# Kernel tuning notes

Measured on AMD Instinct MI355X. Metric: run time of the kernel, lower is better.

## Reference

```python
import jax, jax.numpy as jnp
import numpy as np

# ---- config (CSA layer, layer_idx=0 of pattern 'CSA,HCA') ----
B, T, C = 2, 2048, 2048
NH, NKV = 16, 8
HD = C // NH            # 128 head dim
ROPE_DIM = HD // 2      # partial RoPE dims (rope_head_dim=0 default)
RATIO = 4               # csa_compress_ratio
G = T // RATIO          # compressed groups (T divisible by ratio -> no pad)
IDX_NH = NH
IDX_HD = max(8, C // NH // 2)  # 64
TOPK = 64               # index_topk
Q_RANK = C // 2         # _default_rank
O_RPG = C // 2          # o_proj rank_per_group, o_groups=1


def rms_norm(x, eps=1e-6):
    return x * jax.lax.rsqrt(jnp.mean(jnp.square(x), axis=-1, keepdims=True) + eps)


def _rope(x, cos, sin):
    d = x.shape[-1] // 2
    x1, x2 = x[..., :d], x[..., d:]
    return jnp.concatenate([x1 * cos + x2 * sin, -x1 * sin + x2 * cos], axis=-1)


def partial_rope(x, cos, sin):
    # rotate only the last ROPE_DIM dims; cos/sin: [..., ROPE_DIM//2]
    xn, xr = x[..., :-ROPE_DIM], x[..., -ROPE_DIM:]
    return jnp.concatenate([xn, _rope(xr, cos, sin)], axis=-1)


def setup_inputs() -> dict:
    key = jax.random.key(0)
    ks = jax.random.split(key, 16)
    s = 0.02
    x = jax.random.normal(ks[0], (B, T, C), jnp.float32)
    pos = jnp.arange(T, dtype=jnp.float32)
    inv = 10000.0 ** (-jnp.arange(0, HD // 2, dtype=jnp.float32) / (HD // 2))
    ang = pos[:, None] * inv[None, :]  # [T, HD//2]
    p = lambda i, shp: jax.random.normal(ks[i], shp, jnp.float32) * s
    return dict(
        x=x, cos=jnp.cos(ang), sin=jnp.sin(ang),
        q_a_w=p(1, (C, Q_RANK)), q_b_w=p(2, (Q_RANK, NH * HD)),
        ck_w=p(3, (C, NKV * HD)), cv_w=p(4, (C, NKV * HD)), cg_w=p(5, (C, NKV * HD)),
        c_ape=p(6, (RATIO, NKV, HD)),
        iq_w=p(7, (C, IDX_NH * IDX_HD)), ik_w=p(8, (C, IDX_NH * IDX_HD)),
        ig_w=p(9, (C, IDX_NH * IDX_HD)), i_ape=p(10, (RATIO, IDX_NH, IDX_HD)),
        sink=jnp.zeros((NH,), jnp.float32),
        o_wa=p(11, (1, O_RPG, C)), o_pb=p(12, (O_RPG, C)),
    )


def reference(x, cos, sin, q_a_w, q_b_w, ck_w, cv_w, cg_w, c_ape,
              iq_w, ik_w, ig_w, i_ape, sink, o_wa, o_pb):
    NEG = jnp.finfo(jnp.float32).min
    half = ROPE_DIM // 2
    # --- low-rank queries + partial RoPE ---
    q = (x @ q_a_w @ q_b_w).reshape(B, T, NH, HD)
    q = partial_rope(q, cos[None, :, None, :half], sin[None, :, None, :half])
    # --- GatedCompressor: learned gated pooling over blocks of RATIO ---
    k = (x @ ck_w).reshape(B, G, RATIO, NKV, HD)
    v = (x @ cv_w).reshape(B, G, RATIO, NKV, HD)
    g = (x @ cg_w).reshape(B, G, RATIO, NKV, HD) + c_ape[None, None]
    w = jax.nn.softmax(g, axis=2)
    ck = (k * w).sum(2)  # [B,G,NKV,HD]
    cv = (v * w).sum(2)
    group_ends = jnp.arange(RATIO - 1, T, RATIO)  # [G]
    ckr = partial_rope(ck, cos[group_ends][None, :, None, :half],
                       sin[group_ends][None, :, None, :half])
    # --- LightningIndexer: compressed indexer keys + per-token top-k groups ---
    ik = (x @ ik_w).reshape(B, G, RATIO, IDX_NH, IDX_HD)
    ig = (x @ ig_w).reshape(B, G, RATIO, IDX_NH, IDX_HD) + i_ape[None, None]
    iw = jax.nn.softmax(ig, axis=2)
    ikeys = rms_norm((ik * iw).sum(2))  # [B,G,IH,IHD]
    iq = rms_norm((x @ iq_w).reshape(B, T, IDX_NH, IDX_HD))
    iscore = jnp.einsum('bthd,bghd->bhtg', iq, ikeys) * IDX_HD ** -0.5
    iscore = iscore.mean(axis=1)  # [B,T,G]
    causal = group_ends[None, None, :] <= jnp.arange(T)[None, :, None]
    iscore = jnp.where(causal, iscore, NEG)
    sel = jax.lax.top_k(iscore, TOPK)[1]  # [B,T,K]
    bidx = jnp.arange(B)[:, None, None]
    tidx = jnp.arange(T)[None, :, None]
    mask = jnp.zeros((B, T, G), bool).at[bidx, tidx, sel].set(True) & causal
    # --- compressed sparse attention with sink, GQA expand ---
    rep = NH // NKV
    kk = jnp.repeat(ckr, rep, axis=2)  # [B,G,NH,HD]
    vv = jnp.repeat(cv, rep, axis=2)
    scores = jnp.einsum('bthd,bghd->bhtg', q, kk) * HD ** -0.5
    scores = jnp.where(mask[:, None], scores, NEG)
    sinkb = jnp.broadcast_to(sink.reshape(1, NH, 1, 1), (B, NH, T, 1))
    probs = jax.nn.softmax(jnp.concatenate([scores, sinkb], axis=-1), axis=-1)[..., :-1]
    out = jnp.einsum('bhtg,bghd->bthd', probs, vv).reshape(B, T, C)
    # --- GroupedOutputProjection (o_groups=1) ---
    h = jnp.einsum('btgd,grd->btgr', out.reshape(B, T, 1, C), o_wa).reshape(B, T, -1)
    return rms_norm(h) @ o_pb
```

## Files before the change

### kernel.cpp

```cpp
#include <hip/hip_runtime.h>
#include <hip/hip_bf16.h>
#include <math.h>

constexpr int Bn  = 2;
constexpr int Tn  = 2048;
constexpr int NHn = 16;
constexpr int NKVn= 8;
constexpr int Gn  = 512;
constexpr int TKn = 64;

typedef __attribute__((ext_vector_type(8))) __bf16 bf16x8;
typedef __attribute__((ext_vector_type(4))) __bf16 bf16x4;
typedef __attribute__((ext_vector_type(2))) __bf16 bf16x2;
typedef __attribute__((ext_vector_type(4))) float f32x4;

__device__ __forceinline__ void gload_lds16(const void* g, void* l) {
  __builtin_amdgcn_global_load_lds(
      (const __attribute__((address_space(1))) unsigned int*)g,
      (__attribute__((address_space(3))) unsigned int*)l, 16, 0, 0);
}

__global__ __launch_bounds__(512) void gemm_kvqa_8ph(
    const __bf16* __restrict__ A, const __bf16* __restrict__ Bt,
    float* __restrict__ Cf, __bf16* __restrict__ Cq)
{
  constexpr int K = 2048;
  constexpr int NT = K / 64;
  __shared__ __bf16 lds[2][2][2][256][32];
  const int tid = threadIdx.x;
  const int wid = tid >> 6, lane = tid & 63;
  const int wm = wid >> 2, wn = wid & 3;
  const int row0 = blockIdx.y * 256, col0 = blockIdx.x * 256;

  f32x4 acc[8][4];
  const f32x4 zero = {0.f, 0.f, 0.f, 0.f};
  #pragma unroll
  for (int i = 0; i < 8; ++i)
    #pragma unroll
    for (int j = 0; j < 4; ++j) acc[i][j] = zero;

  auto stage1 = [&](int kt, int op, int ph, int buf) {
    long k0 = (long)kt * 64 + ph * 32;
    const __bf16* src = op ? Bt : A;
    const int base0 = op ? col0 : row0;
    #pragma unroll
    for (int l = 0; l < 2; ++l) {
      int u = l * 512 + tid;
      int r = u >> 2, c4 = u & 3;
      long csrc = (long)((c4 ^ ((r >> 1) & 3)) * 8);
      gload_lds16(src + (long)(base0 + r) * K + k0 + csrc, &lds[buf][op][ph][r][c4 * 8]);
    }
  };

  stage1(0, 0, 0, 0);
  stage1(0, 1, 0, 0);
  stage1(0, 0, 1, 0);
  stage1(0, 1, 1, 0);
  asm volatile("s_waitcnt vmcnt(4)" ::: "memory");
  asm volatile("s_barrier" ::: "memory");

  for (int kt = 0; kt < NT; ++kt) {
    const int buf = kt & 1;
    const bool pre = (kt + 1 < NT);
    bf16x8 afA[4], afB[4], bf[4];

    #pragma unroll
    for (int i = 0; i < 4; ++i) {
      int r = wm * 128 + i * 16 + (lane & 15);
      int c4 = (lane >> 4) ^ ((r >> 1) & 3);
      afA[i] = *(const bf16x8*)&lds[buf][0][0][r][c4 * 8];
    }
    #pragma unroll
    for (int i = 0; i < 4; ++i) {
      int r = wn * 64 + i * 16 + (lane & 15);
      int c4 = (lane >> 4) ^ ((r >> 1) & 3);
      bf[i] = *(const bf16x8*)&lds[buf][1][0][r][c4 * 8];
    }
    if (pre) stage1(kt + 1, 0, 0, buf ^ 1);
    asm volatile("s_barrier" ::: "memory");
    asm volatile("s_waitcnt lgkmcnt(0)" ::: "memory");
    __builtin_amdgcn_sched_barrier(0);
    __builtin_amdgcn_s_setprio(1);
    #pragma unroll
    for (int i = 0; i < 4; ++i)
      #pragma unroll
      for (int j = 0; j < 4; ++j)
        acc[i][j] = __builtin_amdgcn_mfma_f32_16x16x32_bf16(afA[i], bf[j], acc[i][j], 0, 0, 0);
    __builtin_amdgcn_s_setprio(0);
    asm volatile("s_barrier" ::: "memory");

    #pragma unroll
    for (int i = 0; i < 4; ++i) {
      int r = wm * 128 + (i + 4) * 16 + (lane & 15);
      int c4 = (lane >> 4) ^ ((r >> 1) & 3);
      afB[i] = *(const bf16x8*)&lds[buf][0][0][r][c4 * 8];
    }
    if (pre) {
      stage1(kt + 1, 1, 0, buf ^ 1);
      asm volatile("s_waitcnt vmcnt(4)" ::: "memory");
    } else {
      asm volatile("s_waitcnt vmcnt(0)" ::: "memory");
    }
    asm volatile("s_barrier" ::: "memory");
    asm volatile("s_waitcnt lgkmcnt(0)" ::: "memory");
    __builtin_amdgcn_sched_barrier(0);
    __builtin_amdgcn_s_setprio(1);
    #pragma unroll
    for (int i = 0; i < 4; ++i)
      #pragma unroll
      for (int j = 0; j < 4; ++j)
        acc[i + 4][j] = __builtin_amdgcn_mfma_f32_16x16x32_bf16(afB[i], bf[j], acc[i + 4][j], 0, 0, 0);
    __builtin_amdgcn_s_setprio(0);
    asm volatile("s_barrier" ::: "memory");

    #pragma unroll
    for (int i = 0; i < 4; ++i) {
      int r = wm * 128 + i * 16 + (lane & 15);
      int c4 = (lane >> 4) ^ ((r >> 1) & 3);
      afA[i] = *(const bf16x8*)&lds[buf][0][1][r][c4 * 8];
    }
    #pragma unroll
    for (int i = 0; i < 4; ++i) {
      int r = wn * 64 + i * 16 + (lane & 15);
      int c4 = (lane >> 4) ^ ((r >> 1) & 3);
      bf[i] = *(const bf16x8*)&lds[buf][1][1][r][c4 * 8];
    }
    if (pre) stage1(kt + 1, 0, 1, buf ^ 1);
    asm volatile("s_barrier" ::: "memory");
    asm volatile("s_waitcnt lgkmcnt(0)" ::: "memory");
    __builtin_amdgcn_sched_barrier(0);
    __builtin_amdgcn_s_setprio(1);
    #pragma unroll
    for (int i = 0; i < 4; ++i)
      #pragma unroll
      for (int j = 0; j < 4; ++j)
        acc[i][j] = __builtin_amdgcn_mfma_f32_16x16x32_bf16(afA[i], bf[j], acc[i][j], 0, 0, 0);
    __builtin_amdgcn_s_setprio(0);
    asm volatile("s_barrier" ::: "memory");

    #pragma unroll
    for (int i = 0; i < 4; ++i) {
      int r = wm * 128 + (i + 4) * 16 + (lane & 15);
      int c4 = (lane >> 4) ^ ((r >> 1) & 3);
      afB[i] = *(const bf16x8*)&lds[buf][0][1][r][c4 * 8];
    }
    if (pre) {
      stage1(kt + 1, 1, 1, buf ^ 1);
      asm volatile("s_waitcnt vmcnt(4)" ::: "memory");
    }
    asm volatile("s_barrier" ::: "memory");
    asm volatile("s_waitcnt lgkmcnt(0)" ::: "memory");
    __builtin_amdgcn_sched_barrier(0);
    __builtin_amdgcn_s_setprio(1);
    #pragma unroll
    for (int i = 0; i < 4; ++i)
      #pragma unroll
      for (int j = 0; j < 4; ++j)
        acc[i + 4][j] = __builtin_amdgcn_mfma_f32_16x16x32_bf16(afB[i], bf[j], acc[i + 4][j], 0, 0, 0);
    __builtin_amdgcn_s_setprio(0);
    asm volatile("s_barrier" ::: "memory");
  }

  const int crow = (lane >> 4) * 4, ccol = lane & 15;
  const bool isQ = (col0 >= 3072);
  #pragma unroll
  for (int mf = 0; mf < 8; ++mf)
    #pragma unroll
    for (int nf = 0; nf < 4; ++nf)
      #pragma unroll
      for (int j = 0; j < 4; ++j) {
        long r = row0 + wm * 128 + mf * 16 + crow + j;
        long c = col0 + wn * 64 + nf * 16 + ccol;
        float v = acc[mf][nf][j];
        if (isQ) Cq[r * 1024 + (c - 3072)] = (__bf16)v;
        else     Cf[r * 3072 + c] = v;
      }
}

__global__ __launch_bounds__(512) void gemm_split_8ph(
    const __bf16* __restrict__ Ah, const __bf16* __restrict__ Al,
    const __bf16* __restrict__ Bh, const __bf16* __restrict__ Bl,
    float* __restrict__ C, int M, int N, int K, float alpha)
{
  const int NT = K >> 5;
  constexpr int LA_H = 0;
  constexpr int LA_L = 8192;
  constexpr int LB_H = 16384;
  constexpr int LBUF = 28672;
  __shared__ __bf16 sm[2 * LBUF];
  const int tid = threadIdx.x;
  const int wid = tid >> 6, lane = tid & 63;
  const int wm = wid >> 2, wn = wid & 3;
  const int row0 = blockIdx.y * 256, col0 = blockIdx.x * 192;

  f32x4 acc[8][3];
  const f32x4 zero = {0.f, 0.f, 0.f, 0.f};
  #pragma unroll
  for (int i = 0; i < 8; ++i)
    #pragma unroll
    for (int j = 0; j < 3; ++j) acc[i][j] = zero;

  auto stageA = [&](int kt, int buf, int which) {
    long k0 = (long)kt * 32;
    const __bf16* src = which ? Al : Ah;
    __bf16* dst = &sm[buf * LBUF + (which ? LA_L : LA_H)];
    #pragma unroll
    for (int l = 0; l < 2; ++l) {
      int u = l * 512 + tid;
      int r = u >> 2, c4 = u & 3;
      long csrc = (long)((c4 ^ ((r >> 1) & 3)) * 8);
      gload_lds16(src + (long)(row0 + r) * K + k0 + csrc, dst + u * 8);
    }
  };
  auto stageB = [&](int kt, int buf) {
    long k0 = (long)kt * 32;
    __bf16* dst = &sm[buf * LBUF + LB_H];
    #pragma unroll
    for (int l = 0; l < 3; ++l) {
      int u = l * 512 + tid;
      int v = (u < 768) ? u : u - 768;
      const __bf16* src = (u < 768) ? Bh : Bl;
      int r = v >> 2, c4 = v & 3;
      long csrc = (long)((c4 ^ ((r >> 1) & 3)) * 8);
      gload_lds16(src + (long)(col0 + r) * K + k0 + csrc, dst + u * 8);
    }
  };

  stageB(0, 0);
  stageA(0, 0, 0);
  stageA(0, 0, 1);
  asm volatile("s_waitcnt vmcnt(2)" ::: "memory");
  asm volatile("s_barrier" ::: "memory");

  for (int kt = 0; kt < NT; ++kt) {
    const int buf = kt & 1;
    const bool pre = (kt + 1 < NT);
    bf16x8 a_h[4], a_l[4], b_h[3], b_l[3];

    #pragma unroll
    for (int i = 0; i < 4; ++i) {
      int r = wm * 128 + i * 16 + (lane & 15);
      int c4 = (lane >> 4) ^ ((r >> 1) & 3);
      a_h[i] = *(const bf16x8*)&sm[buf * LBUF + LA_H + r * 32 + c4 * 8];
    }
    #pragma unroll
    for (int j = 0; j < 3; ++j) {
      int r = wn * 48 + j * 16 + (lane & 15);
      int c4 = (lane >> 4) ^ ((r >> 1) & 3);
      b_h[j] = *(const bf16x8*)&sm[buf * LBUF + LB_H + r * 32 + c4 * 8];
    }
    if (pre) {
      stageB(kt + 1, buf ^ 1);
      asm volatile("s_waitcnt vmcnt(3)" ::: "memory");
    } else {
      asm volatile("s_waitcnt vmcnt(0)" ::: "memory");
    }
    asm volatile("s_barrier" ::: "memory");
    asm volatile("s_waitcnt lgkmcnt(0)" ::: "memory");
    __builtin_amdgcn_sched_barrier(0);
    __builtin_amdgcn_s_setprio(1);
    #pragma unroll
    for (int i = 0; i < 4; ++i)
      #pragma unroll
      for (int j = 0; j < 3; ++j)
        acc[i][j] = __builtin_amdgcn_mfma_f32_16x16x32_bf16(a_h[i], b_h[j], acc[i][j], 0, 0, 0);
    __builtin_amdgcn_s_setprio(0);
    asm volatile("s_barrier" ::: "memory");

    #pragma unroll
    for (int i = 0; i < 4; ++i) {
      int r = wm * 128 + i * 16 + (lane & 15);
      int c4 = (lane >> 4) ^ ((r >> 1) & 3);
      a_l[i] = *(const bf16x8*)&sm[buf * LBUF + LA_L + r * 32 + c4 * 8];
    }
    #pragma unroll
    for (int j = 0; j < 3; ++j) {
      int r = wn * 48 + j * 16 + (lane & 15);
      int c4 = (lane >> 4) ^ ((r >> 1) & 3);
      b_l[j] = *(const bf16x8*)&sm[buf * LBUF + LB_H + 6144 + r * 32 + c4 * 8];
    }
    if (pre) stageA(kt + 1, buf ^ 1, 0);
    asm volatile("s_barrier" ::: "memory");
    asm volatile("s_waitcnt lgkmcnt(0)" ::: "memory");
    __builtin_amdgcn_sched_barrier(0);
    __builtin_amdgcn_s_setprio(1);
    #pragma unroll
    for (int i = 0; i < 4; ++i)
      #pragma unroll
      for (int j = 0; j < 3; ++j) {
        acc[i][j] = __builtin_amdgcn_mfma_f32_16x16x32_bf16(a_h[i], b_l[j], acc[i][j], 0, 0, 0);
        acc[i][j] = __builtin_amdgcn_mfma_f32_16x16x32_bf16(a_l[i], b_h[j], acc[i][j], 0, 0, 0);
      }
    __builtin_amdgcn_s_setprio(0);
    asm volatile("s_barrier" ::: "memory");

    #pragma unroll
    for (int i = 0; i < 4; ++i) {
      int r = wm * 128 + (i + 4) * 16 + (lane & 15);
      int c4 = (lane >> 4) ^ ((r >> 1) & 3);
      a_h[i] = *(const bf16x8*)&sm[buf * LBUF + LA_H + r * 32 + c4 * 8];
    }
    if (pre) stageA(kt + 1, buf ^ 1, 1);
    asm volatile("s_barrier" ::: "memory");
    asm volatile("s_waitcnt lgkmcnt(0)" ::: "memory");
    __builtin_amdgcn_sched_barrier(0);
    __builtin_amdgcn_s_setprio(1);
    #pragma unroll
    for (int i = 0; i < 4; ++i)
      #pragma unroll
      for (int j = 0; j < 3; ++j)
        acc[i + 4][j] = __builtin_amdgcn_mfma_f32_16x16x32_bf16(a_h[i], b_h[j], acc[i + 4][j], 0, 0, 0);
    __builtin_amdgcn_s_setprio(0);
    asm volatile("s_barrier" ::: "memory");

    #pragma unroll
    for (int i = 0; i < 4; ++i) {
      int r = wm * 128 + (i + 4) * 16 + (lane & 15);
      int c4 = (lane >> 4) ^ ((r >> 1) & 3);
      a_l[i] = *(const bf16x8*)&sm[buf * LBUF + LA_L + r * 32 + c4 * 8];
    }
    if (pre)
      asm volatile("s_waitcnt vmcnt(2)" ::: "memory");
    asm volatile("s_barrier" ::: "memory");
    asm volatile("s_waitcnt lgkmcnt(0)" ::: "memory");
    __builtin_amdgcn_sched_barrier(0);
    __builtin_amdgcn_s_setprio(1);
    #pragma unroll
    for (int i = 0; i < 4; ++i)
      #pragma unroll
      for (int j = 0; j < 3; ++j) {
        acc[i + 4][j] = __builtin_amdgcn_mfma_f32_16x16x32_bf16(a_h[i], b_l[j], acc[i + 4][j], 0, 0, 0);
        acc[i + 4][j] = __builtin_amdgcn_mfma_f32_16x16x32_bf16(a_l[i], b_h[j], acc[i + 4][j], 0, 0, 0);
      }
    __builtin_amdgcn_s_setprio(0);
    asm volatile("s_barrier" ::: "memory");
  }

  const int crow = (lane >> 4) * 4, ccol = lane & 15;
  #pragma unroll
  for (int mf = 0; mf < 8; ++mf)
    #pragma unroll
    for (int nf = 0; nf < 3; ++nf)
      #pragma unroll
      for (int j = 0; j < 4; ++j) {
        long r = row0 + wm * 128 + mf * 16 + crow + j;
        long c = col0 + wn * 48 + nf * 16 + ccol;
        C[r * N + c] = acc[mf][nf][j] * alpha;
      }
}

template<int EPI>
__global__ __launch_bounds__(256) void gemm_pipe(
    const __bf16* __restrict__ A, const __bf16* __restrict__ Bt,
    void* __restrict__ Cp, int N, int K,
    const float* __restrict__ cosb, const float* __restrict__ sinb,
    const float* __restrict__ rs)
{
  const int NT = K >> 6;
  __shared__ __bf16 lds[2][2][2][128][32];
  const int tid = threadIdx.x;
  const int wid = tid >> 6, lane = tid & 63;
  const int wm = wid >> 1, wn = wid & 1;
  const int row0 = blockIdx.y * 128, col0 = blockIdx.x * 128;

  f32x4 acc[4][4];
  const f32x4 zero = {0.f, 0.f, 0.f, 0.f};
  #pragma unroll
  for (int i = 0; i < 4; ++i)
    #pragma unroll
    for (int j = 0; j < 4; ++j) acc[i][j] = zero;

  auto stage = [&](int kt, int p, int buf) {
    long k0 = (long)kt * 64 + p * 32;
    #pragma unroll
    for (int l = 0; l < 2; ++l) {
      int u = l * 256 + tid;
      int r = u >> 2, c4 = u & 3;
      long csrc = (long)((c4 ^ ((r >> 1) & 3)) * 8);
      gload_lds16(A  + (long)(row0 + r) * K + k0 + csrc, &lds[buf][0][p][r][c4 * 8]);
      gload_lds16(Bt + (long)(col0 + r) * K + k0 + csrc, &lds[buf][1][p][r][c4 * 8]);
    }
  };

  stage(0, 0, 0);
  stage(0, 1, 0);

  for (int kt = 0; kt < NT; ++kt) {
    const int buf = kt & 1;
    #pragma unroll
    for (int ph = 0; ph < 2; ++ph) {
      if (kt + 1 < NT) {
        stage(kt + 1, ph, buf ^ 1);
        asm volatile("s_waitcnt vmcnt(8)" ::: "memory");
      } else {
        if (ph == 0) asm volatile("s_waitcnt vmcnt(4)" ::: "memory");
        else         asm volatile("s_waitcnt vmcnt(0)" ::: "memory");
      }
      asm volatile("s_barrier" ::: "memory");
      bf16x8 af[4], bfr[4];
      #pragma unroll
      for (int mf = 0; mf < 4; ++mf) {
        int r = wm * 64 + mf * 16 + (lane & 15);
        int c4 = (lane >> 4) ^ ((r >> 1) & 3);
        af[mf] = *(const bf16x8*)&lds[buf][0][ph][r][c4 * 8];
      }
      #pragma unroll
      for (int nf = 0; nf < 4; ++nf) {
        int r = wn * 64 + nf * 16 + (lane & 15);
        int c4 = (lane >> 4) ^ ((r >> 1) & 3);
        bfr[nf] = *(const bf16x8*)&lds[buf][1][ph][r][c4 * 8];
      }
      __builtin_amdgcn_s_setprio(1);
      #pragma unroll
      for (int mf = 0; mf < 4; ++mf)
        #pragma unroll
        for (int nf = 0; nf < 4; ++nf)
          acc[mf][nf] = __builtin_amdgcn_mfma_f32_16x16x32_bf16(af[mf], bfr[nf], acc[mf][nf], 0, 0, 0);
      __builtin_amdgcn_s_setprio(0);
      asm volatile("s_barrier" ::: "memory");
    }
  }

  const int crow = (lane >> 4) * 4, ccol = lane & 15;
  if constexpr (EPI == 1) {
    __bf16* C = (__bf16*)Cp;
    if (wn == 1) {
      #pragma unroll
      for (int mf = 0; mf < 4; ++mf)
        #pragma unroll
        for (int j = 0; j < 4; ++j) {
          long r = row0 + wm * 64 + mf * 16 + crow + j;
          int t = (int)(r & 2047);
          #pragma unroll
          for (int nfp = 0; nfp < 2; ++nfp) {
            int jj = nfp * 16 + ccol;
            float c = cosb[t * 64 + jj], s = sinb[t * 64 + jj];
            float x1 = acc[mf][nfp][j];
            float x2 = acc[mf][nfp + 2][j];
            C[r * N + col0 + 64 + jj] = (__bf16)(x1 * c + x2 * s);
            C[r * N + col0 + 96 + jj] = (__bf16)(-x1 * s + x2 * c);
          }
        }
    } else {
      #pragma unroll
      for (int mf = 0; mf < 4; ++mf)
        #pragma unroll
        for (int nf = 0; nf < 4; ++nf)
          #pragma unroll
          for (int j = 0; j < 4; ++j) {
            long r = row0 + wm * 64 + mf * 16 + crow + j;
            long c = col0 + nf * 16 + ccol;
            C[r * N + c] = (__bf16)acc[mf][nf][j];
          }
    }
  } else {
    #pragma unroll
    for (int mf = 0; mf < 4; ++mf)
      #pragma unroll
      for (int nf = 0; nf < 4; ++nf)
        #pragma unroll
        for (int j = 0; j < 4; ++j) {
          long r = row0 + wm * 64 + mf * 16 + crow + j;
          long c = col0 + wn * 64 + nf * 16 + ccol;
          float v = acc[mf][nf][j];
          if constexpr (EPI == 2)
            ((float*)Cp)[r * N + c] = v * rs[r];
          else
            ((__bf16*)Cp)[r * N + c] = (__bf16)v;
        }
  }
}

__global__ __launch_bounds__(256) void gemm_split(
    const __bf16* __restrict__ Ah, const __bf16* __restrict__ Al,
    const __bf16* __restrict__ Bh, const __bf16* __restrict__ Bl,
    float* __restrict__ C, int M, int N, int K, float alpha,
    long sA, long sB, long sC)
{
  const int NT = K >> 5;
  __shared__ __bf16 lds[2][4][128][32];
  const int tid = threadIdx.x;
  const int wid = tid >> 6, lane = tid & 63;
  const int wm = wid >> 1, wn = wid & 1;
  const int row0 = blockIdx.y * 128, col0 = blockIdx.x * 128;
  Ah += (long)blockIdx.z * sA;  Al += (long)blockIdx.z * sA;
  Bh += (long)blockIdx.z * sB;  Bl += (long)blockIdx.z * sB;

  f32x4 acc[4][4];
  const f32x4 zero = {0.f, 0.f, 0.f, 0.f};
  #pragma unroll
  for (int i = 0; i < 4; ++i)
    #pragma unroll
    for (int j = 0; j < 4; ++j) acc[i][j] = zero;

  auto stage = [&](int kt, int buf) {
    long k0 = (long)kt * 32;
    #pragma unroll
    for (int l = 0; l < 2; ++l) {
      int u = l * 256 + tid;
      int r = u >> 2, c4 = u & 3;
      long csrc = (long)((c4 ^ ((r >> 1) & 3)) * 8);
      long ga = (long)(row0 + r) * K + k0 + csrc;
      long gb = (long)(col0 + r) * K + k0 + csrc;
      gload_lds16(Ah + ga, &lds[buf][0][r][c4 * 8]);
      gload_lds16(Al + ga, &lds[buf][1][r][c4 * 8]);
      gload_lds16(Bh + gb, &lds[buf][2][r][c4 * 8]);
      gload_lds16(Bl + gb, &lds[buf][3][r][c4 * 8]);
    }
  };

  stage(0, 0);

  for (int kt = 0; kt < NT; ++kt) {
    const int buf = kt & 1;
    if (kt + 1 < NT) {
      stage(kt + 1, buf ^ 1);
      asm volatile("s_waitcnt vmcnt(8)" ::: "memory");
    } else {
      asm volatile("s_waitcnt vmcnt(0)" ::: "memory");
    }
    asm volatile("s_barrier" ::: "memory");
    bf16x8 ah[4], al[4], bh[4], bl[4];
    #pragma unroll
    for (int mf = 0; mf < 4; ++mf) {
      int r = wm * 64 + mf * 16 + (lane & 15);
      int c4 = (lane >> 4) ^ ((r >> 1) & 3);
      ah[mf] = *(const bf16x8*)&lds[buf][0][r][c4 * 8];
      al[mf] = *(const bf16x8*)&lds[buf][1][r][c4 * 8];
    }
    #pragma unroll
    for (int nf = 0; nf < 4; ++nf) {
      int r = wn * 64 + nf * 16 + (lane & 15);
      int c4 = (lane >> 4) ^ ((r >> 1) & 3);
      bh[nf] = *(const bf16x8*)&lds[buf][2][r][c4 * 8];
      bl[nf] = *(const bf16x8*)&lds[buf][3][r][c4 * 8];
    }
    __builtin_amdgcn_s_setprio(1);
    #pragma unroll
    for (int mf = 0; mf < 4; ++mf)
      #pragma unroll
      for (int nf = 0; nf < 4; ++nf) {
        acc[mf][nf] = __builtin_amdgcn_mfma_f32_16x16x32_bf16(ah[mf], bh[nf], acc[mf][nf], 0, 0, 0);
        acc[mf][nf] = __builtin_amdgcn_mfma_f32_16x16x32_bf16(ah[mf], bl[nf], acc[mf][nf], 0, 0, 0);
        acc[mf][nf] = __builtin_amdgcn_mfma_f32_16x16x32_bf16(al[mf], bh[nf], acc[mf][nf], 0, 0, 0);
      }
    __builtin_amdgcn_s_setprio(0);
    asm volatile("s_barrier" ::: "memory");
  }

  const int crow = (lane >> 4) * 4, ccol = lane & 15;
  #pragma unroll
  for (int mf = 0; mf < 4; ++mf)
    #pragma unroll
    for (int nf = 0; nf < 4; ++nf)
      #pragma unroll
      for (int j = 0; j < 4; ++j) {
        long r = row0 + wm * 64 + mf * 16 + crow + j;
        long c = col0 + wn * 64 + nf * 16 + ccol;
        C[(long)blockIdx.z * sC + r * N + c] = acc[mf][nf][j] * alpha;
      }
}

__global__ __launch_bounds__(256) void prep_index(
    const float* __restrict__ x,
    const float* __restrict__ s0, const float* __restrict__ s1,
    const float* __restrict__ s2,
    __bf16* __restrict__ hiB, __bf16* __restrict__ loB, long dstride,
    __bf16* __restrict__ xhi, __bf16* __restrict__ xlo)
{
  __shared__ float tile[64][65];
  int z = blockIdx.y;
  int tid = threadIdx.x;
  if (z < 3) {
    const int R = 2048, Cc = 1024;
    const float* in = (z == 0) ? s0 : (z == 1) ? s1 : s2;
    __bf16* hiT = hiB + (long)z * dstride;
    __bf16* loT = loB + (long)z * dstride;
    int f = blockIdx.x;
    int r0 = (f >> 4) * 64, c0 = (f & 15) * 64;
    #pragma unroll
    for (int j = 0; j < 16; ++j) {
      int idx = tid + j * 256;
      int r = idx >> 6, c = idx & 63;
      tile[r][c] = in[(long)(r0 + r) * Cc + c0 + c];
    }
    __syncthreads();
    #pragma unroll
    for (int j = 0; j < 16; ++j) {
      int idx = tid + j * 256;
      int c = idx >> 6, r = idx & 63;
      float v = tile[r][c];
      __bf16 h = (__bf16)v;
      hiT[(long)(c0 + c) * R + r0 + r] = h;
      loT[(long)(c0 + c) * R + r0 + r] = (__bf16)(v - (float)h);
    }
  } else {
    for (long i = ((long)blockIdx.x * 256 + tid) * 4; i < 8388608; i += 524288) {
      float4 v = *(const float4*)&x[i];
      bf16x4 h, l;
      h[0] = (__bf16)v.x; l[0] = (__bf16)(v.x - (float)h[0]);
      h[1] = (__bf16)v.y; l[1] = (__bf16)(v.y - (float)h[1]);
      h[2] = (__bf16)v.z; l[2] = (__bf16)(v.z - (float)h[2]);
      h[3] = (__bf16)v.w; l[3] = (__bf16)(v.w - (float)h[3]);
      *(bf16x4*)&xhi[i] = h;
      *(bf16x4*)&xlo[i] = l;
    }
  }
}

__global__ __launch_bounds__(256) void prep_main(
    const float* __restrict__ s0, const float* __restrict__ s1,
    const float* __restrict__ s2, const float* __restrict__ s3,
    const float* __restrict__ s4, const float* __restrict__ s5,
    const float* __restrict__ wa,
    __bf16* __restrict__ W, long W2, __bf16* __restrict__ owab)
{
  __shared__ float tile[64][65];
  int z = blockIdx.y;
  int tid = threadIdx.x;
  if (z < 6) {
    int R, Cc, r0, c0;
    const float* in;
    if (z < 4) {
      R = 2048; Cc = 1024;
      in = (z == 0) ? s0 : (z == 1) ? s1 : (z == 2) ? s2 : s3;
      r0 = (blockIdx.x >> 4) * 64; c0 = (blockIdx.x & 15) * 64;
    } else {
      R = 1024; Cc = 2048;
      in = (z == 4) ? s4 : s5;
      r0 = (blockIdx.x >> 5) * 64; c0 = (blockIdx.x & 31) * 64;
    }
    __bf16* out = W + (long)z * W2;
    #pragma unroll
    for (int j = 0; j < 16; ++j) {
      int idx = tid + j * 256;
      int r = idx >> 6, c = idx & 63;
      tile[r][c] = in[(long)(r0 + r) * Cc + c0 + c];
    }
    __syncthreads();
    #pragma unroll
    for (int j = 0; j < 16; ++j) {
      int idx = tid + j * 256;
      int c = idx >> 6, r = idx & 63;
      out[(long)(c0 + c) * R + r0 + r] = (__bf16)tile[r][c];
    }
  } else {
    for (long i = ((long)blockIdx.x * 256 + tid) * 4; i < 2097152; i += 524288) {
      float4 v = *(const float4*)&wa[i];
      bf16x4 o;
      o[0] = (__bf16)v.x; o[1] = (__bf16)v.y; o[2] = (__bf16)v.z; o[3] = (__bf16)v.w;
      *(bf16x4*)&owab[i] = o;
    }
  }
}

__global__ __launch_bounds__(256) void reduce_ckcv(
    const float* __restrict__ base, const float* __restrict__ c_ape,
    const float* __restrict__ cosb, const float* __restrict__ sinb,
    __bf16* __restrict__ ckb, __bf16* __restrict__ cvb)
{
  __shared__ float sck[256];
  const long S = 3072;
  int tid = threadIdx.x;
  int c = blockIdx.x * 256 + tid;
  int g = blockIdx.y, b = blockIdx.z;
  long row0 = (long)b * Tn + 4 * g;
  float lg[4], mx = -1e30f;
  #pragma unroll
  for (int r = 0; r < 4; ++r) {
    lg[r] = base[(row0 + r) * S + 2048 + c] + c_ape[r * 1024 + c];
    mx = fmaxf(mx, lg[r]);
  }
  float ssum = 0.f;
  #pragma unroll
  for (int r = 0; r < 4; ++r) { lg[r] = expf(lg[r] - mx); ssum += lg[r]; }
  float inv = 1.f / ssum, ak = 0.f, av = 0.f;
  #pragma unroll
  for (int r = 0; r < 4; ++r) {
    float w = lg[r] * inv;
    ak = fmaf(base[(row0 + r) * S + c],        w, ak);
    av = fmaf(base[(row0 + r) * S + 1024 + c], w, av);
  }
  long o = ((long)b * Gn + g) * 1024 + c;
  cvb[o] = (__bf16)av;
  sck[tid] = ak;
  __syncthreads();
  int d = c & 127;
  float outk = ak;
  if (d >= 64) {
    int t = 4 * g + 3;
    if (d < 96) {
      int j = d - 64;
      outk = ak * cosb[t * 64 + j] + sck[tid + 32] * sinb[t * 64 + j];
    } else {
      int j = d - 96;
      outk = -sck[tid - 32] * sinb[t * 64 + j] + ak * cosb[t * 64 + j];
    }
  }
  ckb[o] = (__bf16)outk;
}

__global__ __launch_bounds__(1024) void reduce_idx_fused(
    const float* __restrict__ base, const float* __restrict__ i_ape,
    __bf16* __restrict__ khi, __bf16* __restrict__ klo,
    __bf16* __restrict__ qhi, __bf16* __restrict__ qlo)
{
  const long S = 3072;
  int tid = threadIdx.x;
  int bid = blockIdx.x;
  if (bid < Gn * Bn) {
    int g = bid & (Gn - 1), b = bid >> 9;
    long row0 = (long)b * Tn + 4 * g;
    float lg[4], mx = -1e30f;
    #pragma unroll
    for (int r = 0; r < 4; ++r) {
      lg[r] = base[(row0 + r) * S + 1024 + tid] + i_ape[r * 1024 + tid];
      mx = fmaxf(mx, lg[r]);
    }
    float ssum = 0.f;
    #pragma unroll
    for (int r = 0; r < 4; ++r) { lg[r] = expf(lg[r] - mx); ssum += lg[r]; }
    float inv = 1.f / ssum, red = 0.f;
    #pragma unroll
    for (int r = 0; r < 4; ++r) red = fmaf(base[(row0 + r) * S + tid], lg[r] * inv, red);
    float ss = red * red;
    #pragma unroll
    for (int o = 32; o; o >>= 1) ss += __shfl_xor(ss, o);
    float v = red * rsqrtf(ss * (1.f / 64.f) + 1e-6f);
    long oi = ((long)b * Gn + g) * 1024 + tid;
    __bf16 h = (__bf16)v;
    khi[oi] = h; klo[oi] = (__bf16)(v - (float)h);
  } else {
    long row = bid - Gn * Bn;
    float v = base[row * S + 2048 + tid];
    float ss = v * v;
    #pragma unroll
    for (int o = 32; o; o >>= 1) ss += __shfl_xor(ss, o);
    float y = v * rsqrtf(ss * (1.f / 64.f) + 1e-6f);
    __bf16 h = (__bf16)y;
    qhi[row * 1024 + tid] = h;
    qlo[row * 1024 + tid] = (__bf16)(y - (float)h);
  }
}

__global__ __launch_bounds__(256) void rms_scales(
    const __bf16* __restrict__ h, float* __restrict__ rs)
{
  int wid = threadIdx.x >> 6, lane = threadIdx.x & 63;
  long row = (long)blockIdx.x * 4 + wid;
  const __bf16* hr = h + row * 1024 + lane * 16;
  bf16x8 a = *(const bf16x8*)hr;
  bf16x8 b = *(const bf16x8*)(hr + 8);
  float ss = 0.f;
  #pragma unroll
  for (int j = 0; j < 8; ++j) {
    float x = (float)a[j], y = (float)b[j];
    ss = fmaf(x, x, ss); ss = fmaf(y, y, ss);
  }
  #pragma unroll
  for (int o = 1; o < 64; o <<= 1) ss += __shfl_xor(ss, o);
  if (lane == 0) rs[row] = rsqrtf(ss * (1.f / 1024.f) + 1e-6f);
}

__global__ __launch_bounds__(256) void topk_kernel(
    const float* __restrict__ iscore, int* __restrict__ selidx, int* __restrict__ selcnt)
{
  int wave = threadIdx.x >> 6, lane = threadIdx.x & 63;
  long bt = (long)blockIdx.x * 4 + wave;
  int t = (int)(bt % Tn);
  const float* row = iscore + bt * Gn;
  int ng = (t + 1) >> 2; if (ng > Gn) ng = Gn;
  int cap = ng < TKn ? ng : TKn;
  float s[8];
  #pragma unroll
  for (int j = 0; j < 8; ++j) {
    int g = lane + 64 * j;
    s[j] = (g < ng) ? row[g] : -INFINITY;
  }
  int* outp = selidx + bt * TKn;
  for (int it = 0; it < cap; ++it) {
    float bv = -INFINITY; int bi = Gn;
    #pragma unroll
    for (int j = 0; j < 8; ++j) {
      int g = lane + 64 * j;
      if (s[j] > bv) { bv = s[j]; bi = g; }
    }
    #pragma unroll
    for (int o = 1; o < 64; o <<= 1) {
      float ov = __shfl_xor(bv, o); int oi = __shfl_xor(bi, o);
      if (ov > bv || (ov == bv && oi < bi)) { bv = ov; bi = oi; }
    }
    if (lane == 0) outp[it] = bi;
    #pragma unroll
    for (int j = 0; j < 8; ++j) if (bi == lane + 64 * j) s[j] = -INFINITY;
  }
  for (int it = cap + lane; it < TKn; it += 64) outp[it] = 0;
  if (lane == 0) selcnt[bt] = cap;
}

__global__ __launch_bounds__(256) void attn_kernel(
    const __bf16* __restrict__ q, const __bf16* __restrict__ ckb,
    const __bf16* __restrict__ cvb, const int* __restrict__ selidx,
    const int* __restrict__ selcnt, const float* __restrict__ sink,
    __bf16* __restrict__ out)
{
  __shared__ float sS[4][16][68];
  __shared__ int   sG[4][64];
  const float scale = 0.08838834764831845f;
  int wid = threadIdx.x >> 6, lane = threadIdx.x & 63;
  long bt = (long)blockIdx.x * 4 + wid;
  int b = (int)(bt >> 11);
  int cnt = selcnt[bt];
  int gid = (lane < cnt) ? selidx[bt * TKn + lane] : 0;
  sG[wid][lane] = gid;

  int grp = lane >> 3;
  int sub = lane & 7;
  int h0 = grp * 2, h1 = h0 + 1;
  int d0 = sub * 16;

  const __bf16* qrow = q + bt * 2048;
  float q0[16], q1[16];
  {
    bf16x8 a0 = *(const bf16x8*)&qrow[h0 * 128 + d0];
    bf16x8 a1 = *(const bf16x8*)&qrow[h0 * 128 + d0 + 8];
    bf16x8 c0 = *(const bf16x8*)&qrow[h1 * 128 + d0];
    bf16x8 c1 = *(const bf16x8*)&qrow[h1 * 128 + d0 + 8];
    #pragma unroll
    for (int j = 0; j < 8; ++j) {
      q0[j] = (float)a0[j]; q0[8 + j] = (float)a1[j];
      q1[j] = (float)c0[j]; q1[8 + j] = (float)c1[j];
    }
  }
  __syncthreads();

  for (int i0 = 0; i0 < 64; i0 += 8) {
    #pragma unroll
    for (int u = 0; u < 8; ++u) {
      int i = i0 + u;
      int g = sG[wid][i];
      const __bf16* kr = ckb + ((long)(b * Gn + g)) * 1024 + lane * 16;
      bf16x8 k0 = *(const bf16x8*)kr;
      bf16x8 k1 = *(const bf16x8*)(kr + 8);
      float p0 = 0.f, p1 = 0.f;
      #pragma unroll
      for (int j = 0; j < 8; ++j) {
        float kv = (float)k0[j];
        p0 = fmaf(kv, q0[j], p0); p1 = fmaf(kv, q1[j], p1);
      }
      #pragma unroll
      for (int j = 0; j < 8; ++j) {
        float kv = (float)k1[j];
        p0 = fmaf(kv, q0[8 + j], p0); p1 = fmaf(kv, q1[8 + j], p1);
      }
      p0 += __shfl_xor(p0, 1); p0 += __shfl_xor(p0, 2); p0 += __shfl_xor(p0, 4);
      p1 += __shfl_xor(p1, 1); p1 += __shfl_xor(p1, 2); p1 += __shfl_xor(p1, 4);
      if (sub == 0) { sS[wid][h0][i] = p0; sS[wid][h1][i] = p1; }
    }
  }
  __syncthreads();

  {
    int h = lane >> 2, qtr = lane & 3;
    float sv[16];
    float mx = -INFINITY;
    #pragma unroll
    for (int j = 0; j < 16; ++j) {
      int i = qtr * 16 + j;
      float s = (i < cnt) ? sS[wid][h][i] * scale : -INFINITY;
      sv[j] = s; mx = fmaxf(mx, s);
    }
    mx = fmaxf(mx, __shfl_xor(mx, 1));
    mx = fmaxf(mx, __shfl_xor(mx, 2));
    float snk = sink[h];
    mx = fmaxf(mx, snk);
    float sum = 0.f;
    #pragma unroll
    for (int j = 0; j < 16; ++j) { sv[j] = __expf(sv[j] - mx); sum += sv[j]; }
    sum += __shfl_xor(sum, 1);
    sum += __shfl_xor(sum, 2);
    sum += __expf(snk - mx);
    float inv = 1.f / sum;
    #pragma unroll
    for (int j = 0; j < 16; ++j) sS[wid][h][qtr * 16 + j] = sv[j] * inv;
  }
  __syncthreads();

  float o0[16], o1[16];
  #pragma unroll
  for (int j = 0; j < 16; ++j) { o0[j] = 0.f; o1[j] = 0.f; }
  for (int i0 = 0; i0 < 64; i0 += 8) {
    #pragma unroll
    for (int u = 0; u < 8; ++u) {
      int i = i0 + u;
      int g = sG[wid][i];
      float p0 = sS[wid][h0][i], p1 = sS[wid][h1][i];
      const __bf16* vr = cvb + ((long)(b * Gn + g)) * 1024 + lane * 16;
      bf16x8 v0 = *(const bf16x8*)vr;
      bf16x8 v1 = *(const bf16x8*)(vr + 8);
      #pragma unroll
      for (int j = 0; j < 8; ++j) {
        float vv = (float)v0[j];
        o0[j] = fmaf(p0, vv, o0[j]); o1[j] = fmaf(p1, vv, o1[j]);
      }
      #pragma unroll
      for (int j = 0; j < 8; ++j) {
        float vv = (float)v1[j];
        o0[8 + j] = fmaf(p0, vv, o0[8 + j]); o1[8 + j] = fmaf(p1, vv, o1[8 + j]);
      }
    }
  }
  __bf16* ob = out + bt * 2048;
  bf16x8 w;
  #pragma unroll
  for (int j = 0; j < 8; ++j) w[j] = (__bf16)o0[j];
  *(bf16x8*)&ob[h0 * 128 + d0] = w;
  #pragma unroll
  for (int j = 0; j < 8; ++j) w[j] = (__bf16)o0[8 + j];
  *(bf16x8*)&ob[h0 * 128 + d0 + 8] = w;
  #pragma unroll
  for (int j = 0; j < 8; ++j) w[j] = (__bf16)o1[j];
  *(bf16x8*)&ob[h1 * 128 + d0] = w;
  #pragma unroll
  for (int j = 0; j < 8; ++j) w[j] = (__bf16)o1[8 + j];
  *(bf16x8*)&ob[h1 * 128 + d0 + 8] = w;
}

extern "C" void kernel_launch(void* const* d_in, const int* in_sizes, int n_in,
                              void* d_out, int out_size, void* d_ws, size_t ws_size,
                              hipStream_t stream) {
  const float* x     = (const float*)d_in[0];
  const float* cosb  = (const float*)d_in[1];
  const float* sinb  = (const float*)d_in[2];
  const float* q_a_w = (const float*)d_in[3];
  const float* q_b_w = (const float*)d_in[4];
  const float* ck_w  = (const float*)d_in[5];
  const float* cv_w  = (const float*)d_in[6];
  const float* cg_w  = (const float*)d_in[7];
  const float* c_ape = (const float*)d_in[8];
  const float* iq_w  = (const float*)d_in[9];
  const float* ik_w  = (const float*)d_in[10];
  const float* ig_w  = (const float*)d_in[11];
  const float* i_ape = (const float*)d_in[12];
  const float* sink  = (const float*)d_in[13];
  const float* o_wa  = (const float*)d_in[14];
  const float* o_pb  = (const float*)d_in[15];
  float* outp = (float*)d_out;
  float* ws = (float*)d_ws;

  const long F  = 4194304;
  const long M1 = 1048576;

  float* b_all = ws;
  float*  iscore = ws + F;
  __bf16* oatt_b = (__bf16*)(ws + F);
  __bf16* hb_b   = (__bf16*)ws;

  __bf16* iq_hi = (__bf16*)d_out;
  __bf16* iq_lo = (__bf16*)d_out + 4194304;
  __bf16* qb    = (__bf16*)d_out;

  char* tp = (char*)(ws + 3 * F);
  __bf16* ckb = (__bf16*)tp;     tp += (size_t)M1 * 4;
  __bf16* cvb = (__bf16*)tp;     tp += (size_t)M1 * 4;
  int*   selidx = (int*)tp;      tp += 2097152;
  int*   selcnt = selidx + Bn * Tn * TKn;
  __bf16* ikeys_hi = (__bf16*)tp; tp += 2097152;
  __bf16* ikeys_lo = (__bf16*)tp; tp += 2097152;
  __bf16* xhi = (__bf16*)tp;      tp += 16777216;
  __bf16* xlo = (__bf16*)tp;      tp += 16777216;
  __bf16* W   = (__bf16*)tp;      tp += 7 * 4194304;
  __bf16* qa_buf = (__bf16*)tp;   tp += 8388608;
  float*  rs     = (float*)tp;    tp += 16384;
  const long W2 = 2097152;
  __bf16* Whi = W;            __bf16* Wlo = W + 3 * W2;
  __bf16* ckT  = W;
  __bf16* qbT  = W + 4*W2;
  __bf16* opbT = W + 5*W2;   __bf16* owab = W + 6*W2;

  prep_index<<<dim3(512, 4), 256, 0, stream>>>(
      x, ik_w, ig_w, iq_w, Whi, Wlo, W2, xhi, xlo);

  gemm_split_8ph<<<dim3(16, 16), 512, 0, stream>>>(xhi, xlo, Whi, Wlo, b_all,
      4096, 3072, 2048, 1.f);
  reduce_idx_fused<<<dim3(Gn * Bn + Bn * Tn), 1024, 0, stream>>>(
      b_all, i_ape, ikeys_hi, ikeys_lo, iq_hi, iq_lo);

  gemm_split<<<dim3(4, 16, 2), 256, 0, stream>>>(iq_hi, iq_lo, ikeys_hi, ikeys_lo, iscore,
      2048, 512, 1024, 1.f / 128.f, (long)2048 * 1024, (long)512 * 1024, (long)2048 * 512);
  topk_kernel<<<dim3(Bn * Tn / 4), 256, 0, stream>>>(iscore, selidx, selcnt);

  prep_main<<<dim3(512, 7), 256, 0, stream>>>(
      ck_w, cv_w, cg_w, q_a_w, q_b_w, o_pb, o_wa, W, W2, owab);

  gemm_kvqa_8ph<<<dim3(16, 16), 512, 0, stream>>>(xhi, ckT, b_all, qa_buf);
  reduce_ckcv<<<dim3(4, Gn, Bn), 256, 0, stream>>>(b_all, c_ape, cosb, sinb, ckb, cvb);

  gemm_pipe<1><<<dim3(16, 32), 256, 0, stream>>>(
      qa_buf, qbT, qb, 2048, 1024, cosb, sinb, nullptr);

  attn_kernel<<<dim3(Bn * Tn / 4), 256, 0, stream>>>(qb, ckb, cvb, selidx, selcnt, sink, oatt_b);

  gemm_pipe<0><<<dim3(8, 32), 256, 0, stream>>>(
      oatt_b, owab, hb_b, 1024, 2048, nullptr, nullptr, nullptr);
  rms_scales<<<dim3(1024), 256, 0, stream>>>(hb_b, rs);
  gemm_pipe<2><<<dim3(16, 32), 256, 0, stream>>>(
      hb_b, opbT, outp, 2048, 1024, nullptr, nullptr, rs);
}
```

Measured before the change: 500.5 us.

## Restructure split-bf16 GEMM K-loop into three full-tile MFMA phases

The main loop of the split-precision (hi/lo bf16) GEMM changes from four half-tile phases to three phases that each cover all 8 M-fragments: hi*hi, hi*lo, then lo*hi. Prefetch staging for the next K tile is regrouped, with B and the first A half issued together and the vmcnt waits retuned. The aim is fewer barriers per K step and longer uninterrupted MFMA bursts. The cost is more live A-fragment registers (8 hi plus 8 lo), which could raise register pressure or cause spills, and the changed wait counts could reorder loads against the barriers.

Result: no change. 502.1 us (+0.3%).

```diff
diff --git a/kernel.cpp b/kernel.cpp
--- a/kernel.cpp
+++ b/kernel.cpp
@@ -235,10 +235,10 @@
   for (int kt = 0; kt < NT; ++kt) {
     const int buf = kt & 1;
     const bool pre = (kt + 1 < NT);
-    bf16x8 a_h[4], a_l[4], b_h[3], b_l[3];
-
-    #pragma unroll
-    for (int i = 0; i < 4; ++i) {
+    bf16x8 a_h[8], a_l[8], b_h[3], b_l[3];
+
+    #pragma unroll
+    for (int i = 0; i < 8; ++i) {
       int r = wm * 128 + i * 16 + (lane & 15);
       int c4 = (lane >> 4) ^ ((r >> 1) & 3);
       a_h[i] = *(const bf16x8*)&sm[buf * LBUF + LA_H + r * 32 + c4 * 8];
@@ -251,16 +251,14 @@
     }
     if (pre) {
       stageB(kt + 1, buf ^ 1);
-      asm volatile("s_waitcnt vmcnt(3)" ::: "memory");
-    } else {
-      asm volatile("s_waitcnt vmcnt(0)" ::: "memory");
+      stageA(kt + 1, buf ^ 1, 0);
     }
     asm volatile("s_barrier" ::: "memory");
     asm volatile("s_waitcnt lgkmcnt(0)" ::: "memory");
     __builtin_amdgcn_sched_barrier(0);
     __builtin_amdgcn_s_setprio(1);
     #pragma unroll
-    for (int i = 0; i < 4; ++i)
+    for (int i = 0; i < 8; ++i)
       #pragma unroll
       for (int j = 0; j < 3; ++j)
         acc[i][j] = __builtin_amdgcn_mfma_f32_16x16x32_bf16(a_h[i], b_h[j], acc[i][j], 0, 0, 0);
@@ -268,70 +266,46 @@
     asm volatile("s_barrier" ::: "memory");
 
     #pragma unroll
-    for (int i = 0; i < 4; ++i) {
-      int r = wm * 128 + i * 16 + (lane & 15);
-      int c4 = (lane >> 4) ^ ((r >> 1) & 3);
-      a_l[i] = *(const bf16x8*)&sm[buf * LBUF + LA_L + r * 32 + c4 * 8];
-    }
-    #pragma unroll
     for (int j = 0; j < 3; ++j) {
       int r = wn * 48 + j * 16 + (lane & 15);
       int c4 = (lane >> 4) ^ ((r >> 1) & 3);
       b_l[j] = *(const bf16x8*)&sm[buf * LBUF + LB_H + 6144 + r * 32 + c4 * 8];
     }
-    if (pre) stageA(kt + 1, buf ^ 1, 0);
+    if (pre)
+      asm volatile("s_waitcnt vmcnt(5)" ::: "memory");
+    else
+      asm volatile("s_waitcnt vmcnt(0)" ::: "memory");
     asm volatile("s_barrier" ::: "memory");
     asm volatile("s_waitcnt lgkmcnt(0)" ::: "memory");
     __builtin_amdgcn_sched_barrier(0);
     __builtin_amdgcn_s_setprio(1);
     #pragma unroll
-    for (int i = 0; i < 4; ++i)
-      #pragma unroll
-      for (int j = 0; j < 3; ++j) {
+    for (int i = 0; i < 8; ++i)
+      #pragma unroll
+      for (int j = 0; j < 3; ++j)
         acc[i][j] = __builtin_amdgcn_mfma_f32_16x16x32_bf16(a_h[i], b_l[j], acc[i][j], 0, 0, 0);
-        acc[i][j] = __builtin_amdgcn_mfma_f32_16x16x32_bf16(a_l[i], b_h[j], acc[i][j], 0, 0, 0);
-      }
     __builtin_amdgcn_s_setprio(0);
     asm volatile("s_barrier" ::: "memory");
 
     #pragma unroll
-    for (int i = 0; i < 4; ++i) {
-      int r = wm * 128 + (i + 4) * 16 + (lane & 15);
-      int c4 = (lane >> 4) ^ ((r >> 1) & 3);
-      a_h[i] = *(const bf16x8*)&sm[buf * LBUF + LA_H + r * 32 + c4 * 8];
-    }
-    if (pre) stageA(kt + 1, buf ^ 1, 1);
+    for (int i = 0; i < 8; ++i) {
+      int r = wm * 128 + i * 16 + (lane & 15);
+      int c4 = (lane >> 4) ^ ((r >> 1) & 3);
+      a_l[i] = *(const bf16x8*)&sm[buf * LBUF + LA_L + r * 32 + c4 * 8];
+    }
+    if (pre) {
+      stageA(kt + 1, buf ^ 1, 1);
+      asm volatile("s_waitcnt vmcnt(2)" ::: "memory");
+    }
     asm volatile("s_barrier" ::: "memory");
     asm volatile("s_waitcnt lgkmcnt(0)" ::: "memory");
     __builtin_amdgcn_sched_barrier(0);
     __builtin_amdgcn_s_setprio(1);
     #pragma unroll
-    for (int i = 0; i < 4; ++i)
+    for (int i = 0; i < 8; ++i)
       #pragma unroll
       for (int j = 0; j < 3; ++j)
-        acc[i + 4][j] = __builtin_amdgcn_mfma_f32_16x16x32_bf16(a_h[i], b_h[j], acc[i + 4][j], 0, 0, 0);
-    __builtin_amdgcn_s_setprio(0);
-    asm volatile("s_barrier" ::: "memory");
-
-    #pragma unroll
-    for (int i = 0; i < 4; ++i) {
-      int r = wm * 128 + (i + 4) * 16 + (lane & 15);
-      int c4 = (lane >> 4) ^ ((r >> 1) & 3);
-      a_l[i] = *(const bf16x8*)&sm[buf * LBUF + LA_L + r * 32 + c4 * 8];
-    }
-    if (pre)
-      asm volatile("s_waitcnt vmcnt(2)" ::: "memory");
-    asm volatile("s_barrier" ::: "memory");
-    asm volatile("s_waitcnt lgkmcnt(0)" ::: "memory");
-    __builtin_amdgcn_sched_barrier(0);
-    __builtin_amdgcn_s_setprio(1);
-    #pragma unroll
-    for (int i = 0; i < 4; ++i)
-      #pragma unroll
-      for (int j = 0; j < 3; ++j) {
-        acc[i + 4][j] = __builtin_amdgcn_mfma_f32_16x16x32_bf16(a_h[i], b_l[j], acc[i + 4][j], 0, 0, 0);
-        acc[i + 4][j] = __builtin_amdgcn_mfma_f32_16x16x32_bf16(a_l[i], b_h[j], acc[i + 4][j], 0, 0, 0);
-      }
+        acc[i][j] = __builtin_amdgcn_mfma_f32_16x16x32_bf16(a_l[i], b_h[j], acc[i][j], 0, 0, 0);
     __builtin_amdgcn_s_setprio(0);
     asm volatile("s_barrier" ::: "memory");
   }
```
